# Kernel tuning notes

Hardware: AMD Instinct MI355X
Metric: run time of the kernel (lower is better)

The kernel has to match this reference:

```python
import jax, jax.numpy as jnp
import numpy as np

B, S, D = 2, 2048, 1280
H = 20
HD = D // H  # 64, rotary dim


def setup_inputs() -> dict:
    key = jax.random.key(0)
    ks = jax.random.split(key, 4)
    scale = 0.02
    return {
        "hidden_states": jax.random.normal(ks[0], (B, S, D), jnp.float32),
        "Wq": jax.random.normal(ks[1], (D, D), jnp.float32) * scale,
        "bq": jnp.zeros((D,), jnp.float32),
        "Wk": jax.random.normal(ks[2], (D, D), jnp.float32) * scale,
        "bk": jnp.zeros((D,), jnp.float32),
        "Wv": jax.random.normal(ks[3], (D, D), jnp.float32) * scale,
        "bv": jnp.zeros((D,), jnp.float32),
    }


def _rotate_half(x):
    x1, x2 = jnp.split(x, 2, axis=-1)
    return jnp.concatenate((-x2, x1), axis=-1)


def _rotary_cos_sin(seq_len, dim, dtype):
    inv_freq = 1.0 / (10000.0 ** (jnp.arange(0, dim, 2, dtype=jnp.float32) / dim))
    t = jnp.arange(seq_len, dtype=jnp.float32)
    freqs = jnp.einsum("i,j->ij", t, inv_freq)          # [S, dim/2]
    emb = jnp.concatenate((freqs, freqs), axis=-1)        # [S, dim]
    return jnp.cos(emb).astype(dtype)[None, None], jnp.sin(emb).astype(dtype)[None, None]


def reference(hidden_states, Wq, bq, Wk, bk, Wv, bv):
    b, s, d = hidden_states.shape
    # QKV projections, split heads -> [B, H, S, HD]
    def proj(W, bias):
        y = hidden_states @ W + bias
        return y.reshape(b, s, H, HD).transpose(0, 2, 1, 3)

    q = proj(Wq, bq) * (HD ** -0.5)  # scale BEFORE rotary, as in source
    k = proj(Wk, bk)
    v = proj(Wv, bv)

    cos, sin = _rotary_cos_sin(s, HD, q.dtype)
    q = q * cos + _rotate_half(q) * sin
    k = k * cos + _rotate_half(k) * sin

    scores = jnp.einsum("bhqd,bhkd->bhqk", q, k)
    probs = jax.nn.softmax(scores, axis=-1)
    ctx = jnp.einsum("bhqk,bhkd->bhqd", probs, v)
    return ctx.transpose(0, 2, 1, 3).reshape(b, s, d)
```

## Files before the change

kernel.cpp:

```cpp
#include <hip/hip_runtime.h>

#define DD 1280
#define SS 2048
#define HH 20

typedef __bf16 bf16x8 __attribute__((ext_vector_type(8)));
typedef float f32x4 __attribute__((ext_vector_type(4)));

typedef __attribute__((address_space(3))) unsigned int lds_uint;
typedef __attribute__((address_space(1))) unsigned int glb_uint;
#define GLL16(g, l) __builtin_amdgcn_global_load_lds((const glb_uint*)(g), (lds_uint*)(l), 16, 0, 0)

__device__ __forceinline__ unsigned short f2bf(float f) {
  union { float f; unsigned u; } v; v.f = f;
  unsigned r = v.u + 0x7fffu + ((v.u >> 16) & 1u);
  return (unsigned short)(r >> 16);
}
__device__ __forceinline__ unsigned f2u(float f) {
  union { float f; unsigned u; } v; v.f = f; return v.u;
}

__global__ __launch_bounds__(256) void prep_kernel(
    const float* __restrict__ X, const float* __restrict__ Wq,
    const float* __restrict__ Wk, const float* __restrict__ Wv,
    unsigned short* __restrict__ Xb, unsigned short* __restrict__ WT,
    float2* __restrict__ cs) {
  __shared__ unsigned short tile[32][33];
  int bid = blockIdx.x, tid = threadIdx.x;
  if (bid < 2560) {
    size_t base = (size_t)bid * 2048 + (size_t)tid * 8;
    const float4* xin = (const float4*)(X + base);
    float4 a = xin[0], c = xin[1];
    ushort4 o0 = make_ushort4(f2bf(a.x), f2bf(a.y), f2bf(a.z), f2bf(a.w));
    ushort4 o1 = make_ushort4(f2bf(c.x), f2bf(c.y), f2bf(c.z), f2bf(c.w));
    *(ushort4*)(Xb + base) = o0;
    *(ushort4*)(Xb + base + 4) = o1;
  } else if (bid < 7360) {
    int wb = bid - 2560;
    int mat = wb / 1600;
    int t = wb % 1600;
    int tn = t % 40, tk = t / 40;
    const float* W = (mat == 0) ? Wq : ((mat == 1) ? Wk : Wv);
    int k0 = tk * 32, n0 = tn * 32;
    int tc = tid & 31, tr = tid >> 5;
#pragma unroll
    for (int i = 0; i < 4; i++) {
      int kl = tr + i * 8;
      tile[kl][tc] = f2bf(W[(size_t)(k0 + kl) * DD + n0 + tc]);
    }
    __syncthreads();
    unsigned short* out = WT + (size_t)mat * DD * DD;
#pragma unroll
    for (int i = 0; i < 4; i++) {
      int nl = tr + i * 8;
      out[(size_t)(n0 + nl) * DD + k0 + tc] = tile[tc][nl];
    }
  } else {
    int idx = (bid - 7360) * 256 + tid;
    int sp = idx >> 5, j = idx & 31;
    float invf = exp2f(-(float)j * 0.41524101186092034f);
    float ang = (float)sp * invf;
    cs[idx] = make_float2(cosf(ang), sinf(ang));
  }
}

__global__ __launch_bounds__(256) void qkv_gemm_kernel(
    const unsigned short* __restrict__ Xb, const unsigned short* __restrict__ WT,
    const float* __restrict__ bq, const float* __restrict__ bk, const float* __restrict__ bv,
    const float2* __restrict__ cs,
    unsigned short* __restrict__ Qr, unsigned short* __restrict__ Kr,
    unsigned short* __restrict__ VT) {
  __shared__ __align__(16) unsigned short As[128 * 32];
  __shared__ __align__(16) unsigned short Bs[128 * 32];
  int bx = blockIdx.x;
  int mat = bx / 320;
  int r0 = bx % 320;
  int tm = r0 / 10, tn = r0 % 10;
  int m0 = tm * 128, n0 = tn * 128;
  int tid = threadIdx.x;
  int lane = tid & 63, wave = tid >> 6;
  int c15 = lane & 15, quad = lane >> 4;
  int wm = wave >> 1, wn = wave & 1;
  const unsigned short* Wm = WT + (size_t)mat * DD * DD;

  int rowA = tid >> 2;
  int c8 = (tid & 3) * 8;
  const unsigned short* gA0 = Xb + (size_t)(m0 + rowA) * DD + c8;
  const unsigned short* gA1 = gA0 + (size_t)64 * DD;
  const unsigned short* gB0 = Wm + (size_t)(n0 + rowA) * DD + c8;
  const unsigned short* gB1 = gB0 + (size_t)64 * DD;
  unsigned short* ldsA0 = As + wave * 512;
  unsigned short* ldsA1 = As + 2048 + wave * 512;
  unsigned short* ldsB0 = Bs + wave * 512;
  unsigned short* ldsB1 = Bs + 2048 + wave * 512;

  f32x4 acc[4][4] = {};

  for (int kk = 0; kk < DD; kk += 32) {
    __syncthreads();
    GLL16(gA0 + kk, ldsA0);
    GLL16(gA1 + kk, ldsA1);
    GLL16(gB0 + kk, ldsB0);
    GLL16(gB1 + kk, ldsB1);
    __syncthreads();
    bf16x8 af[4];
#pragma unroll
    for (int mi = 0; mi < 4; mi++)
      af[mi] = *(const bf16x8*)(As + (wm * 64 + mi * 16 + c15) * 32 + quad * 8);
#pragma unroll
    for (int ni = 0; ni < 4; ni++) {
      bf16x8 bfr = *(const bf16x8*)(Bs + (wn * 64 + ni * 16 + c15) * 32 + quad * 8);
#pragma unroll
      for (int mi = 0; mi < 4; mi++)
        acc[mi][ni] = __builtin_amdgcn_mfma_f32_16x16x32_bf16(af[mi], bfr, acc[mi][ni], 0, 0, 0);
    }
  }

  int growb = m0 + wm * 64;
  int gcolb = n0 + wn * 64;
  if (mat == 2) {
#pragma unroll
    for (int mi = 0; mi < 4; mi++) {
      int row0 = growb + mi * 16 + quad * 4;
      int bb_ = row0 >> 11, sp = row0 & 2047;
#pragma unroll
      for (int ni = 0; ni < 4; ni++) {
        int gcol = gcolb + ni * 16 + c15;
        float bias = bv[gcol];
        int hh = gcol >> 6, dd = gcol & 63;
        f32x4 v = acc[mi][ni];
        ushort4 o = make_ushort4(f2bf(v[0] + bias), f2bf(v[1] + bias),
                                 f2bf(v[2] + bias), f2bf(v[3] + bias));
        *(ushort4*)(VT + ((size_t)((bb_ * HH + hh) * 64 + dd)) * SS + sp) = o;
      }
    }
  } else {
    unsigned short* Out = (mat == 0) ? Qr : Kr;
    const float* bias = (mat == 0) ? bq : bk;
    float qs = (mat == 0) ? 0.18033688011112042f : 1.0f;
#pragma unroll
    for (int mi = 0; mi < 4; mi++) {
      int row0 = growb + mi * 16 + quad * 4;
#pragma unroll
      for (int ni = 0; ni < 2; ni++) {
        int gcol_lo = gcolb + ni * 16 + c15;
        int gcol_hi = gcol_lo + 32;
        float blo = bias[gcol_lo], bhi = bias[gcol_hi];
        int d = ni * 16 + c15;
        f32x4 lo = acc[mi][ni], hi = acc[mi][ni + 2];
#pragma unroll
        for (int r = 0; r < 4; r++) {
          int grow = row0 + r;
          float2 cv = cs[(size_t)(grow & 2047) * 32 + d];
          float xl = (lo[r] + blo) * qs, xh = (hi[r] + bhi) * qs;
          Out[(size_t)grow * DD + gcol_lo] = f2bf(xl * cv.x - xh * cv.y);
          Out[(size_t)grow * DD + gcol_hi] = f2bf(xh * cv.x + xl * cv.y);
        }
      }
    }
  }
}

__device__ __forceinline__ void attn_load_frags(
    bf16x8 (&kf)[2][2], bf16x8 (&vf)[4],
    const unsigned short* Kt, const unsigned short* Vt, int c15, int quad) {
#pragma unroll
  for (int ni = 0; ni < 2; ni++)
#pragma unroll
    for (int kc = 0; kc < 2; kc++)
      kf[ni][kc] = *(const bf16x8*)(Kt + (size_t)(ni * 16 + c15) * DD + kc * 32 + quad * 8);
#pragma unroll
  for (int nio = 0; nio < 4; nio++)
    vf[nio] = *(const bf16x8*)(Vt + (size_t)(nio * 16 + c15) * SS + quad * 8);
}

__device__ __forceinline__ void attn_tile(
    const bf16x8 (&qf)[4][2], const bf16x8 (&kf)[2][2], const bf16x8 (&vf)[4],
    const bf16x8& ones, f32x4 (&of)[4][4], f32x4 (&ol)[4],
    unsigned short* Pw, int c15, int quad) {
  f32x4 sc[4][2] = {};
#pragma unroll
  for (int ni = 0; ni < 2; ni++)
#pragma unroll
    for (int kc = 0; kc < 2; kc++)
#pragma unroll
      for (int mi = 0; mi < 4; mi++)
        sc[mi][ni] = __builtin_amdgcn_mfma_f32_16x16x32_bf16(qf[mi][kc], kf[ni][kc], sc[mi][ni], 0, 0, 0);

  int pos_r = (quad + 2 * ((c15 >> 2) & 3) + (c15 & 3)) & 7;

#define PROD(mi)                                                              \
  {                                                                           \
    _Pragma("unroll")                                                         \
    for (int ni = 0; ni < 2; ni++) {                                          \
      int kc8 = ni * 2 + (c15 >> 3);                                          \
      _Pragma("unroll")                                                       \
      for (int r = 0; r < 4; r++) {                                           \
        unsigned u = f2u(__builtin_amdgcn_exp2f(sc[mi][ni][r]));              \
        int q = (mi) * 16 + quad * 4 + r;                                     \
        int pos = (kc8 + 2 * quad + r) & 7;                                   \
        Pw[q * 64 + pos * 8 + (c15 & 7)] = (unsigned short)(u >> 16);         \
      }                                                                       \
    }                                                                         \
  }
#define CONS(mi)                                                              \
  {                                                                           \
    bf16x8 pf = *(const bf16x8*)(Pw + ((mi) * 16 + c15) * 64 + pos_r * 8);    \
    _Pragma("unroll")                                                         \
    for (int nio = 0; nio < 4; nio++)                                         \
      of[mi][nio] = __builtin_amdgcn_mfma_f32_16x16x32_bf16(pf, vf[nio],      \
                                                            of[mi][nio], 0, 0, 0); \
    ol[mi] = __builtin_amdgcn_mfma_f32_16x16x32_bf16(pf, ones, ol[mi], 0, 0, 0); \
  }

  PROD(0);
  PROD(1); CONS(0);
  PROD(2); CONS(1);
  PROD(3); CONS(2);
  CONS(3);
#undef PROD
#undef CONS
}

__global__ __launch_bounds__(256)
__attribute__((amdgpu_waves_per_eu(2, 4)))
void attn_kernel(
    const unsigned short* __restrict__ Qr, const unsigned short* __restrict__ Kr,
    const unsigned short* __restrict__ VT, float* __restrict__ out) {
  __shared__ __align__(16) unsigned short Pall[4 * 64 * 64];
  __shared__ float Lbuf[64];
  int bx = blockIdx.x;
  int bh = bx % 40, qt = bx / 40;
  int b = bh / HH, h = bh % HH;
  int tid = threadIdx.x;
  int lane = tid & 63, w = tid >> 6;
  int c15 = lane & 15, quad = lane >> 4;
  int q0 = qt * 64;

  const unsigned short* Qbase = Qr + (size_t)(b * SS + q0) * DD + h * 64;
  bf16x8 qf[4][2];
#pragma unroll
  for (int mi = 0; mi < 4; mi++)
#pragma unroll
    for (int kc = 0; kc < 2; kc++)
      qf[mi][kc] = *(const bf16x8*)(Qbase + (size_t)(mi * 16 + c15) * DD + kc * 32 + quad * 8);

  const unsigned short* Kbase = Kr + (size_t)(b * SS + w * 32) * DD + h * 64;
  const unsigned short* Vbase = VT + (size_t)(bh * 64) * SS + w * 32;
  unsigned short* Pw = Pall + w * 4096;

  bf16x8 ones;
#pragma unroll
  for (int i = 0; i < 8; i++) ones[i] = (__bf16)1.0f;

  f32x4 of[4][4] = {};
  f32x4 ol[4] = {};

  bf16x8 kfb[2][2][2], vfb[2][4];
  attn_load_frags(kfb[0], vfb[0], Kbase, Vbase, c15, quad);

  for (int t = 0; t < 16; t += 2) {
    attn_load_frags(kfb[1], vfb[1],
                    Kbase + (size_t)((t + 1) * 128) * DD, Vbase + (t + 1) * 128,
                    c15, quad);
    attn_tile(qf, kfb[0], vfb[0], ones, of, ol, Pw, c15, quad);
    if (t + 2 < 16)
      attn_load_frags(kfb[0], vfb[0],
                      Kbase + (size_t)((t + 2) * 128) * DD, Vbase + (t + 2) * 128,
                      c15, quad);
    attn_tile(qf, kfb[1], vfb[1], ones, of, ol, Pw, c15, quad);
  }

  __syncthreads();
  float* Obuf = (float*)Pall;

  for (int pass = 0; pass < 4; pass++) {
    if (w == pass) {
#pragma unroll
      for (int mi = 0; mi < 4; mi++)
#pragma unroll
        for (int nio = 0; nio < 4; nio++)
#pragma unroll
          for (int r = 0; r < 4; r++) {
            int q = mi * 16 + quad * 4 + r;
            int d = nio * 16 + c15;
            if (pass == 0) Obuf[q * 65 + d] = of[mi][nio][r];
            else           Obuf[q * 65 + d] += of[mi][nio][r];
          }
      if (c15 == 0) {
#pragma unroll
        for (int mi = 0; mi < 4; mi++)
#pragma unroll
          for (int r = 0; r < 4; r++) {
            int q = mi * 16 + quad * 4 + r;
            if (pass == 0) Lbuf[q] = ol[mi][r];
            else           Lbuf[q] += ol[mi][r];
          }
      }
    }
    __syncthreads();
  }

  {
    int row = w * 16 + (lane >> 2);
    int col0 = (lane & 3) * 16;
    float invl = 1.0f / Lbuf[row];
    float* op = out + (size_t)(b * SS + q0 + row) * DD + h * 64 + col0;
    const float* ob = Obuf + row * 65 + col0;
#pragma unroll
    for (int j = 0; j < 4; j++) {
      float4 v = make_float4(ob[j * 4 + 0] * invl, ob[j * 4 + 1] * invl,
                             ob[j * 4 + 2] * invl, ob[j * 4 + 3] * invl);
      *(float4*)(op + j * 4) = v;
    }
  }
}

extern "C" void kernel_launch(void* const* d_in, const int* in_sizes, int n_in,
                              void* d_out, int out_size, void* d_ws, size_t ws_size,
                              hipStream_t stream) {
  (void)in_sizes; (void)n_in; (void)out_size; (void)ws_size;
  const float* X  = (const float*)d_in[0];
  const float* Wq = (const float*)d_in[1];
  const float* bq = (const float*)d_in[2];
  const float* Wk = (const float*)d_in[3];
  const float* bk = (const float*)d_in[4];
  const float* Wv = (const float*)d_in[5];
  const float* bv = (const float*)d_in[6];
  char* ws = (char*)d_ws;
  unsigned short* Xb  = (unsigned short*)(ws);
  unsigned short* WT  = (unsigned short*)(ws + 10485760);
  unsigned short* Qr  = (unsigned short*)(ws + 20316160);
  unsigned short* Kr  = (unsigned short*)(ws + 30801920);
  unsigned short* VTt = (unsigned short*)(ws + 41287680);
  float2* cstab       = (float2*)(ws + 51773440);
  hipLaunchKernelGGL(prep_kernel, dim3(7616), dim3(256), 0, stream, X, Wq, Wk, Wv, Xb, WT, cstab);
  hipLaunchKernelGGL(qkv_gemm_kernel, dim3(960), dim3(256), 0, stream, Xb, WT, bq, bk, bv, cstab, Qr, Kr, VTt);
  hipLaunchKernelGGL(attn_kernel, dim3(1280), dim3(256), 0, stream, Qr, Kr, VTt, (float*)d_out);
}
```

Baseline: 248.2 us.

## Compute transposed scores so exp outputs feed PV MFMA directly from registers

Swaps the operand order of the QK^T MFMA so each lane's score outputs already sit in the A-operand layout needed by the P·V MFMA. The exp results are packed to bf16 in registers, which removes the per-wave LDS round-trip for the probability tile and the separate ones-vector MFMA for row sums. Row sums are kept as scalar register accumulators and reduced across lanes with shuffles at the end. V is loaded as two 4-element pieces to match the permuted key ordering, and the waves_per_eu attribute is dropped, which may change register allocation and occupancy.

```diff
diff --git a/kernel.cpp b/kernel.cpp
--- a/kernel.cpp
+++ b/kernel.cpp
@@ -18,6 +18,9 @@
 }
 __device__ __forceinline__ unsigned f2u(float f) {
   union { float f; unsigned u; } v; v.f = f; return v.u;
+}
+__device__ __forceinline__ float u2f(unsigned x) {
+  union { unsigned u; float f; } v; v.u = x; return v.f;
 }
 
 __global__ __launch_bounds__(256) void prep_kernel(
@@ -161,141 +164,133 @@
   }
 }
 
-__device__ __forceinline__ void attn_load_frags(
-    bf16x8 (&kf)[2][2], bf16x8 (&vf)[4],
-    const unsigned short* Kt, const unsigned short* Vt, int c15, int quad) {
-#pragma unroll
-  for (int ni = 0; ni < 2; ni++)
-#pragma unroll
-    for (int kc = 0; kc < 2; kc++)
-      kf[ni][kc] = *(const bf16x8*)(Kt + (size_t)(ni * 16 + c15) * DD + kc * 32 + quad * 8);
-#pragma unroll
-  for (int nio = 0; nio < 4; nio++)
-    vf[nio] = *(const bf16x8*)(Vt + (size_t)(nio * 16 + c15) * SS + quad * 8);
-}
-
-__device__ __forceinline__ void attn_tile(
-    const bf16x8 (&qf)[4][2], const bf16x8 (&kf)[2][2], const bf16x8 (&vf)[4],
-    const bf16x8& ones, f32x4 (&of)[4][4], f32x4 (&ol)[4],
-    unsigned short* Pw, int c15, int quad) {
-  f32x4 sc[4][2] = {};
-#pragma unroll
-  for (int ni = 0; ni < 2; ni++)
-#pragma unroll
-    for (int kc = 0; kc < 2; kc++)
-#pragma unroll
-      for (int mi = 0; mi < 4; mi++)
-        sc[mi][ni] = __builtin_amdgcn_mfma_f32_16x16x32_bf16(qf[mi][kc], kf[ni][kc], sc[mi][ni], 0, 0, 0);
-
-  int pos_r = (quad + 2 * ((c15 >> 2) & 3) + (c15 & 3)) & 7;
-
-#define PROD(mi)                                                              \
-  {                                                                           \
-    _Pragma("unroll")                                                         \
-    for (int ni = 0; ni < 2; ni++) {                                          \
-      int kc8 = ni * 2 + (c15 >> 3);                                          \
-      _Pragma("unroll")                                                       \
-      for (int r = 0; r < 4; r++) {                                           \
-        unsigned u = f2u(__builtin_amdgcn_exp2f(sc[mi][ni][r]));              \
-        int q = (mi) * 16 + quad * 4 + r;                                     \
-        int pos = (kc8 + 2 * quad + r) & 7;                                   \
-        Pw[q * 64 + pos * 8 + (c15 & 7)] = (unsigned short)(u >> 16);         \
-      }                                                                       \
-    }                                                                         \
-  }
-#define CONS(mi)                                                              \
-  {                                                                           \
-    bf16x8 pf = *(const bf16x8*)(Pw + ((mi) * 16 + c15) * 64 + pos_r * 8);    \
-    _Pragma("unroll")                                                         \
-    for (int nio = 0; nio < 4; nio++)                                         \
-      of[mi][nio] = __builtin_amdgcn_mfma_f32_16x16x32_bf16(pf, vf[nio],      \
-                                                            of[mi][nio], 0, 0, 0); \
-    ol[mi] = __builtin_amdgcn_mfma_f32_16x16x32_bf16(pf, ones, ol[mi], 0, 0, 0); \
-  }
-
-  PROD(0);
-  PROD(1); CONS(0);
-  PROD(2); CONS(1);
-  PROD(3); CONS(2);
-  CONS(3);
-#undef PROD
-#undef CONS
-}
-
 __global__ __launch_bounds__(256)
-__attribute__((amdgpu_waves_per_eu(2, 4)))
 void attn_kernel(
     const unsigned short* __restrict__ Qr, const unsigned short* __restrict__ Kr,
     const unsigned short* __restrict__ VT, float* __restrict__ out) {
-  __shared__ __align__(16) unsigned short Pall[4 * 64 * 64];
+  __shared__ __align__(16) float Obuf[64 * 65];
   __shared__ float Lbuf[64];
   int bx = blockIdx.x;
-  int bh = bx % 40, qt = bx / 40;
+  int bh = bx % 40, qtb = bx / 40;
   int b = bh / HH, h = bh % HH;
   int tid = threadIdx.x;
   int lane = tid & 63, w = tid >> 6;
   int c15 = lane & 15, quad = lane >> 4;
-  int q0 = qt * 64;
-
-  const unsigned short* Qbase = Qr + (size_t)(b * SS + q0) * DD + h * 64;
+  int q0 = qtb * 64;
+
+  const unsigned short* Qb = Qr + (size_t)(b * SS + q0 + c15) * DD + h * 64 + quad * 8;
   bf16x8 qf[4][2];
 #pragma unroll
-  for (int mi = 0; mi < 4; mi++)
-#pragma unroll
-    for (int kc = 0; kc < 2; kc++)
-      qf[mi][kc] = *(const bf16x8*)(Qbase + (size_t)(mi * 16 + c15) * DD + kc * 32 + quad * 8);
-
-  const unsigned short* Kbase = Kr + (size_t)(b * SS + w * 32) * DD + h * 64;
-  const unsigned short* Vbase = VT + (size_t)(bh * 64) * SS + w * 32;
-  unsigned short* Pw = Pall + w * 4096;
-
-  bf16x8 ones;
-#pragma unroll
-  for (int i = 0; i < 8; i++) ones[i] = (__bf16)1.0f;
+  for (int qb = 0; qb < 4; qb++)
+#pragma unroll
+    for (int c = 0; c < 2; c++)
+      qf[qb][c] = *(const bf16x8*)(Qb + (size_t)(qb * 16) * DD + c * 32);
+
+  const unsigned short* Kp = Kr + (size_t)(b * SS + w * 32 + c15) * DD + h * 64 + quad * 8;
+  const unsigned short* Vp = VT + (size_t)(bh * 64 + c15) * SS + w * 32 + quad * 4;
+
+  union bfrag { ushort4 s[2]; bf16x8 v; };
 
   f32x4 of[4][4] = {};
-  f32x4 ol[4] = {};
-
-  bf16x8 kfb[2][2][2], vfb[2][4];
-  attn_load_frags(kfb[0], vfb[0], Kbase, Vbase, c15, quad);
+  float ol[4] = {};
+
+#define LOADK(KF, TT)                                                         \
+  {                                                                           \
+    _Pragma("unroll")                                                         \
+    for (int kb = 0; kb < 2; kb++)                                            \
+      _Pragma("unroll")                                                       \
+      for (int c = 0; c < 2; c++)                                             \
+        KF[kb][c] = *(const bf16x8*)(Kp + (size_t)(TT) * (128 * DD) +         \
+                                     (size_t)(kb * 16) * DD + c * 32);        \
+  }
+#define LOADV(VF, TT)                                                         \
+  {                                                                           \
+    _Pragma("unroll")                                                         \
+    for (int nio = 0; nio < 4; nio++) {                                       \
+      VF[nio].s[0] = *(const ushort4*)(Vp + (size_t)nio * (16 * SS) + (TT) * 128);      \
+      VF[nio].s[1] = *(const ushort4*)(Vp + (size_t)nio * (16 * SS) + (TT) * 128 + 16); \
+    }                                                                         \
+  }
+#define TILE(KF, VF)                                                          \
+  {                                                                           \
+    _Pragma("unroll")                                                         \
+    for (int qb = 0; qb < 4; qb++) {                                          \
+      f32x4 slo = {}, shi = {};                                               \
+      _Pragma("unroll")                                                       \
+      for (int c = 0; c < 2; c++) {                                           \
+        slo = __builtin_amdgcn_mfma_f32_16x16x32_bf16(KF[0][c], qf[qb][c], slo, 0, 0, 0); \
+        shi = __builtin_amdgcn_mfma_f32_16x16x32_bf16(KF[1][c], qf[qb][c], shi, 0, 0, 0); \
+      }                                                                       \
+      unsigned e0 = f2u(__builtin_amdgcn_exp2f(slo[0]));                      \
+      unsigned e1 = f2u(__builtin_amdgcn_exp2f(slo[1]));                      \
+      unsigned e2 = f2u(__builtin_amdgcn_exp2f(slo[2]));                      \
+      unsigned e3 = f2u(__builtin_amdgcn_exp2f(slo[3]));                      \
+      unsigned e4 = f2u(__builtin_amdgcn_exp2f(shi[0]));                      \
+      unsigned e5 = f2u(__builtin_amdgcn_exp2f(shi[1]));                      \
+      unsigned e6 = f2u(__builtin_amdgcn_exp2f(shi[2]));                      \
+      unsigned e7 = f2u(__builtin_amdgcn_exp2f(shi[3]));                      \
+      union { unsigned u[4]; bf16x8 v; } af;                                  \
+      af.u[0] = (e1 & 0xffff0000u) | (e0 >> 16);    \
+      af.u[1] = (e3 & 0xffff0000u) | (e2 >> 16);                              \
+      af.u[2] = (e5 & 0xffff0000u) | (e4 >> 16);                              \
+      af.u[3] = (e7 & 0xffff0000u) | (e6 >> 16);                              \
+          \
+      ol[qb] += u2f(e0 & 0xffff0000u) + u2f(e1 & 0xffff0000u)                 \
+              + u2f(e2 & 0xffff0000u) + u2f(e3 & 0xffff0000u)                 \
+              + u2f(e4 & 0xffff0000u) + u2f(e5 & 0xffff0000u)                 \
+              + u2f(e6 & 0xffff0000u) + u2f(e7 & 0xffff0000u);                \
+      _Pragma("unroll")                                                       \
+      for (int nio = 0; nio < 4; nio++)                                       \
+        of[qb][nio] = __builtin_amdgcn_mfma_f32_16x16x32_bf16(af.v, VF[nio].v, \
+                                                              of[qb][nio], 0, 0, 0); \
+    }                                                                         \
+  }
+
+  bf16x8 kfA[2][2], kfB[2][2];
+  bfrag vfA[4], vfB[4];
+  LOADK(kfA, 0)
+  LOADV(vfA, 0)
 
   for (int t = 0; t < 16; t += 2) {
-    attn_load_frags(kfb[1], vfb[1],
-                    Kbase + (size_t)((t + 1) * 128) * DD, Vbase + (t + 1) * 128,
-                    c15, quad);
-    attn_tile(qf, kfb[0], vfb[0], ones, of, ol, Pw, c15, quad);
-    if (t + 2 < 16)
-      attn_load_frags(kfb[0], vfb[0],
-                      Kbase + (size_t)((t + 2) * 128) * DD, Vbase + (t + 2) * 128,
-                      c15, quad);
-    attn_tile(qf, kfb[1], vfb[1], ones, of, ol, Pw, c15, quad);
-  }
-
-  __syncthreads();
-  float* Obuf = (float*)Pall;
+    LOADK(kfB, t + 1)
+    LOADV(vfB, t + 1)
+    TILE(kfA, vfA)
+    if (t + 2 < 16) {
+      LOADK(kfA, t + 2)
+      LOADV(vfA, t + 2)
+    }
+    TILE(kfB, vfB)
+  }
+#undef LOADK
+#undef LOADV
+#undef TILE
+
+  float lt[4];
+#pragma unroll
+  for (int qb = 0; qb < 4; qb++) {
+    float v = ol[qb];
+    v += __shfl_xor(v, 16);
+    v += __shfl_xor(v, 32);
+    lt[qb] = v;
+  }
 
   for (int pass = 0; pass < 4; pass++) {
     if (w == pass) {
 #pragma unroll
-      for (int mi = 0; mi < 4; mi++)
+      for (int qb = 0; qb < 4; qb++) {
 #pragma unroll
         for (int nio = 0; nio < 4; nio++)
 #pragma unroll
           for (int r = 0; r < 4; r++) {
-            int q = mi * 16 + quad * 4 + r;
+            int q = qb * 16 + quad * 4 + r;
             int d = nio * 16 + c15;
-            if (pass == 0) Obuf[q * 65 + d] = of[mi][nio][r];
-            else           Obuf[q * 65 + d] += of[mi][nio][r];
+            if (pass == 0) Obuf[q * 65 + d] = of[qb][nio][r];
+            else           Obuf[q * 65 + d] += of[qb][nio][r];
           }
-      if (c15 == 0) {
-#pragma unroll
-        for (int mi = 0; mi < 4; mi++)
-#pragma unroll
-          for (int r = 0; r < 4; r++) {
-            int q = mi * 16 + quad * 4 + r;
-            if (pass == 0) Lbuf[q] = ol[mi][r];
-            else           Lbuf[q] += ol[mi][r];
-          }
+        if (quad == 0) {
+          if (pass == 0) Lbuf[qb * 16 + c15] = lt[qb];
+          else           Lbuf[qb * 16 + c15] += lt[qb];
+        }
       }
     }
     __syncthreads();
```

After: 300.3 us. +21.0%, slower.

## Double QKV GEMM K-tile with XOR-swizzled LDS and raise MFMA wave priority

Applied to the files above, without the earlier changes.

The QKV GEMM now stages a 64-wide K slice per iteration instead of 32, which halves the number of barrier pairs. Each wave loads 8-row strips with an XOR swizzle on the 16-byte column chunk, so the LDS fragment reads avoid bank conflicts. In attention, the MFMA sections are wrapped in s_setprio so the waves issuing matrix ops get priority over the softmax/LDS phases of other waves. The larger tile doubles LDS use per block, which may lower occupancy.

```diff
diff --git a/kernel.cpp b/kernel.cpp
--- a/kernel.cpp
+++ b/kernel.cpp
@@ -70,8 +70,8 @@
     const float2* __restrict__ cs,
     unsigned short* __restrict__ Qr, unsigned short* __restrict__ Kr,
     unsigned short* __restrict__ VT) {
-  __shared__ __align__(16) unsigned short As[128 * 32];
-  __shared__ __align__(16) unsigned short Bs[128 * 32];
+  __shared__ __align__(16) unsigned short As[128 * 64];
+  __shared__ __align__(16) unsigned short Bs[128 * 64];
   int bx = blockIdx.x;
   int mat = bx / 320;
   int r0 = bx % 320;
@@ -83,36 +83,39 @@
   int wm = wave >> 1, wn = wave & 1;
   const unsigned short* Wm = WT + (size_t)mat * DD * DD;
 
-  int rowA = tid >> 2;
-  int c8 = (tid & 3) * 8;
-  const unsigned short* gA0 = Xb + (size_t)(m0 + rowA) * DD + c8;
-  const unsigned short* gA1 = gA0 + (size_t)64 * DD;
-  const unsigned short* gB0 = Wm + (size_t)(n0 + rowA) * DD + c8;
-  const unsigned short* gB1 = gB0 + (size_t)64 * DD;
-  unsigned short* ldsA0 = As + wave * 512;
-  unsigned short* ldsA1 = As + 2048 + wave * 512;
-  unsigned short* ldsB0 = Bs + wave * 512;
-  unsigned short* ldsB1 = Bs + 2048 + wave * 512;
+  int srow = lane >> 3;
+  int scol = ((lane & 7) ^ srow) * 8;
+  const unsigned short* gA = Xb + (size_t)(m0 + wave * 8 + srow) * DD + scol;
+  const unsigned short* gB = Wm + (size_t)(n0 + wave * 8 + srow) * DD + scol;
+  unsigned short* ldsA = As + (wave * 8) * 64;
+  unsigned short* ldsB = Bs + (wave * 8) * 64;
 
   f32x4 acc[4][4] = {};
 
-  for (int kk = 0; kk < DD; kk += 32) {
+  for (int kk = 0; kk < DD; kk += 64) {
     __syncthreads();
-    GLL16(gA0 + kk, ldsA0);
-    GLL16(gA1 + kk, ldsA1);
-    GLL16(gB0 + kk, ldsB0);
-    GLL16(gB1 + kk, ldsB1);
+#pragma unroll
+    for (int p = 0; p < 4; p++) {
+      GLL16(gA + (size_t)(p * 32) * DD + kk, ldsA + p * 32 * 64);
+      GLL16(gB + (size_t)(p * 32) * DD + kk, ldsB + p * 32 * 64);
+    }
     __syncthreads();
-    bf16x8 af[4];
-#pragma unroll
-    for (int mi = 0; mi < 4; mi++)
-      af[mi] = *(const bf16x8*)(As + (wm * 64 + mi * 16 + c15) * 32 + quad * 8);
-#pragma unroll
-    for (int ni = 0; ni < 4; ni++) {
-      bf16x8 bfr = *(const bf16x8*)(Bs + (wn * 64 + ni * 16 + c15) * 32 + quad * 8);
-#pragma unroll
-      for (int mi = 0; mi < 4; mi++)
-        acc[mi][ni] = __builtin_amdgcn_mfma_f32_16x16x32_bf16(af[mi], bfr, acc[mi][ni], 0, 0, 0);
+#pragma unroll
+    for (int c = 0; c < 2; c++) {
+      bf16x8 af[4];
+#pragma unroll
+      for (int mi = 0; mi < 4; mi++) {
+        int row = wm * 64 + mi * 16 + c15;
+        af[mi] = *(const bf16x8*)(As + row * 64 + (((c * 4 + quad) ^ (row & 7)) * 8));
+      }
+#pragma unroll
+      for (int ni = 0; ni < 4; ni++) {
+        int rowb = wn * 64 + ni * 16 + c15;
+        bf16x8 bfr = *(const bf16x8*)(Bs + rowb * 64 + (((c * 4 + quad) ^ (rowb & 7)) * 8));
+#pragma unroll
+        for (int mi = 0; mi < 4; mi++)
+          acc[mi][ni] = __builtin_amdgcn_mfma_f32_16x16x32_bf16(af[mi], bfr, acc[mi][ni], 0, 0, 0);
+      }
     }
   }
 
@@ -179,6 +182,7 @@
     const bf16x8& ones, f32x4 (&of)[4][4], f32x4 (&ol)[4],
     unsigned short* Pw, int c15, int quad) {
   f32x4 sc[4][2] = {};
+  __builtin_amdgcn_s_setprio(1);
 #pragma unroll
   for (int ni = 0; ni < 2; ni++)
 #pragma unroll
@@ -186,6 +190,7 @@
 #pragma unroll
       for (int mi = 0; mi < 4; mi++)
         sc[mi][ni] = __builtin_amdgcn_mfma_f32_16x16x32_bf16(qf[mi][kc], kf[ni][kc], sc[mi][ni], 0, 0, 0);
+  __builtin_amdgcn_s_setprio(0);
 
   int pos_r = (quad + 2 * ((c15 >> 2) & 3) + (c15 & 3)) & 7;
 
@@ -206,11 +211,13 @@
 #define CONS(mi)                                                              \
   {                                                                           \
     bf16x8 pf = *(const bf16x8*)(Pw + ((mi) * 16 + c15) * 64 + pos_r * 8);    \
+    __builtin_amdgcn_s_setprio(1);                                            \
     _Pragma("unroll")                                                         \
     for (int nio = 0; nio < 4; nio++)                                         \
       of[mi][nio] = __builtin_amdgcn_mfma_f32_16x16x32_bf16(pf, vf[nio],      \
                                                             of[mi][nio], 0, 0, 0); \
     ol[mi] = __builtin_amdgcn_mfma_f32_16x16x32_bf16(pf, ones, ol[mi], 0, 0, 0); \
+    __builtin_amdgcn_s_setprio(0);                                            \
   }
 
   PROD(0);
```

Result: slower. 278.0 us (+12.0%).
